# Kernel optimization log

Hardware: AMD Instinct MI355X
Metric: run time of the kernel (lower is better)

## Reference

```python
import jax, jax.numpy as jnp
import numpy as np
from jax import lax

B, N, G, K, D = 32, 32768, 64, 32, 384
EPS = 1e-5


def _fps(xyz, npoint):
    # Farthest point sampling; deterministic start at index 0 (original uses randint).
    b, n, _ = xyz.shape
    def step(carry, _):
        distance, farthest = carry
        centroid = jnp.take_along_axis(xyz, farthest[:, None, None], axis=1)  # (B,1,3)
        dist = jnp.sum((xyz - centroid) ** 2, axis=-1)                        # (B,N)
        distance = jnp.minimum(distance, dist)
        new_far = jnp.argmax(distance, axis=-1)
        return (distance, new_far), farthest
    init = (jnp.full((b, n), 1e10, xyz.dtype), jnp.zeros((b,), jnp.int32))
    _, cents = lax.scan(step, init, None, length=npoint)  # (npoint, B)
    return cents.T  # (B, npoint)


def _bn(h, g, bta, m, v):
    # inference-mode BatchNorm over channel (last) dim
    return (h - m) * (g * lax.rsqrt(v + EPS)) + bta


def setup_inputs() -> dict:
    key = jax.random.key(0)
    ks = jax.random.split(key, 5)
    xyz = jax.random.normal(ks[0], (B, N, 3), jnp.float32)
    features = jax.random.normal(ks[1], (B, N, 3), jnp.float32)
    w1 = jax.random.normal(ks[2], (64, 6), jnp.float32) * 0.1
    w2 = jax.random.normal(ks[3], (128, 64), jnp.float32) * 0.1
    w3 = jax.random.normal(ks[4], (D, 128), jnp.float32) * 0.1
    def bn(c):
        return jnp.ones((c,), jnp.float32), jnp.zeros((c,), jnp.float32), jnp.zeros((c,), jnp.float32), jnp.ones((c,), jnp.float32)
    g1, b1, m1, v1 = bn(64)
    g2, b2, m2, v2 = bn(128)
    g3, b3, m3, v3 = bn(D)
    return dict(xyz=xyz, features=features, w1=w1, g1=g1, b1=b1, m1=m1, v1=v1,
                w2=w2, g2=g2, b2=b2, m2=m2, v2=v2, w3=w3, g3=g3, b3=b3, m3=m3, v3=v3)


def reference(xyz, features, w1, g1, b1, m1, v1, w2, g2, b2, m2, v2, w3, g3, b3, m3, v3):
    fps_idx = _fps(xyz, G)                                           # (B,G)
    center = jnp.take_along_axis(xyz, fps_idx[:, :, None], axis=1)   # (B,G,3)
    # KNN via squared distances (same ordering as torch.cdist euclidean)
    xn2 = jnp.sum(xyz * xyz, axis=-1)                                # (B,N)
    cn2 = jnp.sum(center * center, axis=-1)                          # (B,G)
    d2 = cn2[:, :, None] + xn2[:, None, :] - 2.0 * jnp.einsum('bgc,bnc->bgn', center, xyz)
    _, knn_idx = lax.top_k(-d2, K)                                   # (B,G,K)
    gx = jax.vmap(lambda x, i: x[i])(xyz, knn_idx)                   # (B,G,K,3)
    gf = jax.vmap(lambda f, i: f[i])(features, knn_idx)              # (B,G,K,3)
    h = jnp.concatenate([gx - center[:, :, None, :], gf], axis=-1)   # (B,G,K,6)
    h = jax.nn.relu(_bn(jnp.einsum('bgkc,oc->bgko', h, w1), g1, b1, m1, v1))
    h = jax.nn.relu(_bn(jnp.einsum('bgkc,oc->bgko', h, w2), g2, b2, m2, v2))
    h = _bn(jnp.einsum('bgkc,oc->bgko', h, w3), g3, b3, m3, v3)      # (B,G,K,D)
    patch = jnp.max(h, axis=2)                                       # (B,G,D) adaptive max pool
    return center, patch
```

## Files before the change

### kernel.cpp

```cpp
#include <hip/hip_runtime.h>
#include <hip/hip_bf16.h>

#define BB 32
#define NN 32768
#define GG 64
#define KK 32
#define DD 384
#define EPSF 1e-5f
#define FPS_NBLK 8
#define FPS_SL   (NN/FPS_NBLK)

typedef __attribute__((ext_vector_type(8))) short short8;
typedef __attribute__((ext_vector_type(4))) float f32x4;

__device__ __forceinline__ float rn_add(float a, float b){ return __fadd_rn(a,b); }
__device__ __forceinline__ float rn_sub(float a, float b){ return __fsub_rn(a,b); }
__device__ __forceinline__ float rn_mul(float a, float b){ return __fmul_rn(a,b); }

__device__ __forceinline__ unsigned fkey(float d){
  unsigned u = __float_as_uint(d);
  return (u & 0x80000000u) ? ~u : (u | 0x80000000u);
}

__device__ __forceinline__ unsigned short f2bf(float f){
  unsigned u = __float_as_uint(f);
  unsigned r = (u + 0x7FFFu + ((u >> 16) & 1u)) >> 16;
  return (unsigned short)r;
}

#define REP8(X) X(0) X(1) X(2) X(3) X(4) X(5) X(6) X(7)

__device__ float g_center[BB*GG*3];
__device__ int   g_knn[BB*GG*KK];
__device__ float g_w1t[6*64];
__device__ float g_b1[64];
__device__ float g_b2[128];
__device__ float g_b3[384];
__device__ __align__(16) unsigned short g_w2f[8*2*64*8];
__device__ __align__(16) unsigned short g_w3f[24*4*64*8];
__device__ float g_X[BB*NN];
__device__ float g_Y[BB*NN];
__device__ float g_Z[BB*NN];
__device__ float g_N2[BB*NN];
__device__ unsigned long long g_part[BB*FPS_NBLK*GG];

__global__ __launch_bounds__(256) void k_soa(const float* __restrict__ xyz){
  int tid = blockIdx.x * blockDim.x + threadIdx.x;
  int b = tid >> 15;
  int p = tid & (NN - 1);
  const float* s = xyz + (size_t)b*NN*3 + (size_t)p*3;
  float x = s[0], y = s[1], z = s[2];
  g_X[tid] = x;
  g_Y[tid] = y;
  g_Z[tid] = z;
  g_N2[tid] = rn_add(rn_add(rn_mul(x,x), rn_mul(y,y)), rn_mul(z,z));
}

__global__ __launch_bounds__(256) void k_zero(void){
  int tid = blockIdx.x * blockDim.x + threadIdx.x;
  if (tid < BB*FPS_NBLK*GG) g_part[tid] = 0ull;
}

__global__ void k_prep(const float* __restrict__ w1, const float* __restrict__ g1, const float* __restrict__ b1, const float* __restrict__ m1, const float* __restrict__ v1,
                       const float* __restrict__ w2, const float* __restrict__ g2, const float* __restrict__ b2, const float* __restrict__ m2, const float* __restrict__ v2,
                       const float* __restrict__ w3, const float* __restrict__ g3, const float* __restrict__ b3, const float* __restrict__ m3, const float* __restrict__ v3){
  int tid = blockIdx.x * blockDim.x + threadIdx.x;
  int nt  = gridDim.x * blockDim.x;
  for (int e = tid; e < 64*6; e += nt){
    int c = e >> 6, o = e & 63;
    float s = g1[o] * rsqrtf(v1[o] + EPSF);
    g_w1t[e] = w1[o*6 + c] * s;
  }
  for (int o = tid; o < 64; o += nt){
    float s = g1[o] * rsqrtf(v1[o] + EPSF);
    g_b1[o] = b1[o] - m1[o]*s;
  }
  for (int o = tid; o < 128; o += nt){
    float s = g2[o] * rsqrtf(v2[o] + EPSF);
    g_b2[o] = b2[o] - m2[o]*s;
  }
  for (int o = tid; o < 384; o += nt){
    float s = g3[o] * rsqrtf(v3[o] + EPSF);
    g_b3[o] = b3[o] - m3[o]*s;
  }
  for (int idx = tid; idx < 8192; idx += nt){
    int e  = idx & 7;
    int l  = (idx >> 3) & 63;
    int kt = (idx >> 9) & 1;
    int ct = idx >> 10;
    int j  = ct*16 + (l & 15);
    int k  = kt*32 + ((l >> 4) << 3) + e;
    float s = g2[j] * rsqrtf(v2[j] + EPSF);
    g_w2f[idx] = f2bf(w2[j*64 + k] * s);
  }
  for (int idx = tid; idx < 49152; idx += nt){
    int e  = idx & 7;
    int l  = (idx >> 3) & 63;
    int kt = (idx >> 9) & 3;
    int ct = idx >> 11;
    int j  = ct*16 + (l & 15);
    int k  = kt*32 + ((l >> 4) << 3) + e;
    float s = g3[j] * rsqrtf(v3[j] + EPSF);
    g_w3f[idx] = f2bf(w3[j*128 + k] * s);
  }
}

__global__ __launch_bounds__(512)
void k_fps(float* __restrict__ outCenter){
  const int blk = blockIdx.x;
  const int b   = blk & 31;
  const int sub = blk >> 5;
  const int t   = threadIdx.x;
  const int wv  = t >> 6, ln = t & 63;
  const int base = sub * FPS_SL;
  const float* Xb = g_X + (size_t)b*NN;
  const float* Yb = g_Y + (size_t)b*NN;
  const float* Zb = g_Z + (size_t)b*NN;

  __shared__ float sx[FPS_SL], sy[FPS_SL], szz[FPS_SL];
  __shared__ unsigned long long skey[8];
  __shared__ int s_far;

  #pragma unroll
  for (int i = 0; i < 8; ++i){
    int p = (i << 9) + t;
    sx[p]  = Xb[base + p];
    sy[p]  = Yb[base + p];
    szz[p] = Zb[base + p];
  }
  __syncthreads();

#define DD_DECL(i) float dd##i = 1e10f;
  REP8(DD_DECL)
#undef DD_DECL

  int far = 0;
  for (int it = 0; ; ++it){
    if (sub == 0 && t == 0){
      float cx = Xb[far], cy = Yb[far], cz = Zb[far];
      float* cw = g_center  + (size_t)(b*GG + it)*3;
      float* co = outCenter + (size_t)(b*GG + it)*3;
      cw[0] = cx; cw[1] = cy; cw[2] = cz;
      co[0] = cx; co[1] = cy; co[2] = cz;
    }
    if (it == GG - 1) break;

    float cx = Xb[far], cy = Yb[far], cz = Zb[far];
    unsigned long long bk = 0ull;
#define DD_UPD(i) { \
    int p = (i << 9) + t; \
    float dx = rn_sub(sx[p], cx); \
    float dy = rn_sub(sy[p], cy); \
    float dz = rn_sub(szz[p], cz); \
    float s_ = rn_add(rn_add(rn_mul(dx,dx), rn_mul(dy,dy)), rn_mul(dz,dz)); \
    float d_ = fminf(dd##i, s_); \
    dd##i = d_; \
    unsigned long long k_ = ((unsigned long long)fkey(d_) << 32) \
                          | (unsigned)(0xFFFFFFFFu - (unsigned)(base + p)); \
    if (k_ > bk) bk = k_; }
    REP8(DD_UPD)
#undef DD_UPD

    #pragma unroll
    for (int off = 32; off >= 1; off >>= 1){
      unsigned long long o = (unsigned long long)__shfl_xor((long long)bk, off);
      if (o > bk) bk = o;
    }
    if (ln == 0) skey[wv] = bk;
    __syncthreads();
    if (wv == 0){
      unsigned long long m = (ln < 8) ? skey[ln] : 0ull;
      #pragma unroll
      for (int off = 1; off <= 4; off <<= 1){
        unsigned long long o = (unsigned long long)__shfl_xor((long long)m, off);
        if (o > m) m = o;
      }
      if (ln == 0)
        __hip_atomic_store(&g_part[(((b << 3) + sub) << 6) + it], m,
                           __ATOMIC_RELAXED, __HIP_MEMORY_SCOPE_AGENT);
      unsigned long long k = 0ull;
      if (ln < 8){
        unsigned long long* p = &g_part[(((b << 3) + ln) << 6) + it];
        do {
          k = __hip_atomic_load(p, __ATOMIC_RELAXED, __HIP_MEMORY_SCOPE_AGENT);
        } while (k == 0ull);
      }
      #pragma unroll
      for (int off = 1; off <= 4; off <<= 1){
        unsigned long long o = (unsigned long long)__shfl_xor((long long)k, off);
        if (o > k) k = o;
      }
      if (ln == 0) s_far = (int)(0xFFFFFFFFu - (unsigned)(k & 0xFFFFFFFFu));
    }
    __syncthreads();
    far = s_far;
  }
}

__global__ __launch_bounds__(256) void k_knn(void){
  const int bg = blockIdx.x;
  const int b  = bg >> 6;
  const int t  = threadIdx.x;
  const int w  = t >> 6;
  const int ln = t & 63;
  const float4* X4 = (const float4*)(g_X  + (size_t)b*NN);
  const float4* Y4 = (const float4*)(g_Y  + (size_t)b*NN);
  const float4* Z4 = (const float4*)(g_Z  + (size_t)b*NN);
  const float4* N4 = (const float4*)(g_N2 + (size_t)b*NN);

  __shared__ unsigned sE[64];
  __shared__ unsigned long long s_cand[512];
  __shared__ int s_cnt;

  const float* cp = g_center + (size_t)bg*3;
  float cx = cp[0], cy = cp[1], cz = cp[2];
  float cn2 = rn_add(rn_add(rn_mul(cx,cx), rn_mul(cy,cy)), rn_mul(cz,cz));

  float e0 = INFINITY, e1 = INFINITY;
  #pragma unroll 2
  for (int s = 0; s < 32; ++s){
    int q = (s << 8) + t;
    float4 x = X4[q], y = Y4[q], z = Z4[q], n = N4[q];
    #define D2C(c) { \
      float e = rn_add(rn_add(rn_mul(cx,x.c), rn_mul(cy,y.c)), rn_mul(cz,z.c)); \
      float d = rn_sub(rn_add(cn2, n.c), rn_add(e,e)); \
      if (d < e1){ if (d < e0){ e1 = e0; e0 = d; } else e1 = d; } }
    D2C(x) D2C(y) D2C(z) D2C(w)
    #undef D2C
  }

  {
    unsigned v = fkey(e1);
    #pragma unroll
    for (int k = 2; k <= 64; k <<= 1){
      #pragma unroll
      for (int j = k >> 1; j > 0; j >>= 1){
        unsigned o = (unsigned)__shfl_xor((int)v, j);
        bool keepmin = (((ln & k) == 0) == ((ln & j) == 0));
        unsigned mn = o < v ? o : v;
        unsigned mx = o < v ? v : o;
        v = keepmin ? mn : mx;
      }
    }
    if (ln < 16) sE[w*16 + ln] = v;
  }
  if (t == 0) s_cnt = 0;
  __syncthreads();

  unsigned T;
  {
    unsigned v = sE[ln];
    #pragma unroll
    for (int k = 2; k <= 64; k <<= 1){
      #pragma unroll
      for (int j = k >> 1; j > 0; j >>= 1){
        unsigned o = (unsigned)__shfl_xor((int)v, j);
        bool keepmin = (((ln & k) == 0) == ((ln & j) == 0));
        unsigned mn = o < v ? o : v;
        unsigned mx = o < v ? v : o;
        v = keepmin ? mn : mx;
      }
    }
    T = (unsigned)__shfl((int)v, 15);
  }

  #pragma unroll 2
  for (int s = 0; s < 32; ++s){
    int q = (s << 8) + t;
    float4 x = X4[q], y = Y4[q], z = Z4[q], n = N4[q];
    #define COLC(c, kk) { \
      float e = rn_add(rn_add(rn_mul(cx,x.c), rn_mul(cy,y.c)), rn_mul(cz,z.c)); \
      float d = rn_sub(rn_add(cn2, n.c), rn_add(e,e)); \
      unsigned fk = fkey(d); \
      if (fk <= T){ \
        int p = atomicAdd(&s_cnt, 1); \
        if (p < 512) \
          s_cand[p] = ((unsigned long long)fk << 32) | (unsigned)((q<<2)+kk); } }
    COLC(x,0) COLC(y,1) COLC(z,2) COLC(w,3)
    #undef COLC
  }
  __syncthreads();

  if (w == 0){
    int C = s_cnt; if (C > 512) C = 512;
    int* kout = g_knn + (size_t)bg*KK;
    if (C <= 64){
      unsigned long long kk = (ln < C) ? s_cand[ln] : ~0ull;
      #pragma unroll
      for (int k = 2; k <= 64; k <<= 1){
        #pragma unroll
        for (int j = k >> 1; j > 0; j >>= 1){
          unsigned long long o = (unsigned long long)__shfl_xor((long long)kk, j);
          bool keepmin = (((ln & k) == 0) == ((ln & j) == 0));
          unsigned long long mn = o < kk ? o : kk;
          unsigned long long mx = o < kk ? kk : o;
          kk = keepmin ? mn : mx;
        }
      }
      if (ln < KK) kout[ln] = (int)(kk & 0xffffffffu);
    } else {
      unsigned long long md[8];
      #pragma unroll
      for (int j = 0; j < 8; ++j){
        int e = ln + (j << 6);
        md[j] = (e < C) ? s_cand[e] : ~0ull;
      }
      for (int r = 0; r < KK; ++r){
        unsigned long long bk = md[0];
        #pragma unroll
        for (int j = 1; j < 8; ++j) if (md[j] < bk) bk = md[j];
        #pragma unroll
        for (int off = 32; off >= 1; off >>= 1){
          unsigned long long o = (unsigned long long)__shfl_xor((long long)bk, off);
          if (o < bk) bk = o;
        }
        #pragma unroll
        for (int j = 0; j < 8; ++j) if (md[j] == bk) md[j] = ~0ull;
        if (ln == 0) kout[r] = (int)(bk & 0xffffffffu);
      }
    }
  }
}

__global__ __launch_bounds__(256) void k_mlp(const float* __restrict__ xyz,
                                             const float* __restrict__ feat,
                                             float* __restrict__ outPatch){
  const int bg = blockIdx.x;
  const int b  = bg >> 6;
  const int t  = threadIdx.x;
  const int w  = t >> 6;
  const int ln = t & 63;
  const float* xb = xyz  + (size_t)b*NN*3;
  const float* fb = feat + (size_t)b*NN*3;

  __shared__ float h0[KK][8];
  __shared__ __align__(16) unsigned short h1b[KK][72];
  __shared__ __align__(16) unsigned short h2b[KK][136];

  if (t < KK){
    int idx = g_knn[(size_t)bg*KK + t] & (NN - 1);
    const float* cp = g_center + (size_t)bg*3;
    h0[t][0] = rn_sub(xb[idx*3+0], cp[0]);
    h0[t][1] = rn_sub(xb[idx*3+1], cp[1]);
    h0[t][2] = rn_sub(xb[idx*3+2], cp[2]);
    h0[t][3] = fb[idx*3+0];
    h0[t][4] = fb[idx*3+1];
    h0[t][5] = fb[idx*3+2];
  }
  __syncthreads();

  {
    int p = t >> 3, ob = (t & 7) * 8;
    float acc[8];
    #pragma unroll
    for (int j = 0; j < 8; ++j) acc[j] = g_b1[ob + j];
    #pragma unroll
    for (int c = 0; c < 6; ++c){
      float a = h0[p][c];
      const float4* wr = (const float4*)(g_w1t + c*64 + ob);
      float4 wa = wr[0], wb = wr[1];
      acc[0] = fmaf(a, wa.x, acc[0]); acc[1] = fmaf(a, wa.y, acc[1]);
      acc[2] = fmaf(a, wa.z, acc[2]); acc[3] = fmaf(a, wa.w, acc[3]);
      acc[4] = fmaf(a, wb.x, acc[4]); acc[5] = fmaf(a, wb.y, acc[5]);
      acc[6] = fmaf(a, wb.z, acc[6]); acc[7] = fmaf(a, wb.w, acc[7]);
    }
    short8 v;
    #pragma unroll
    for (int j = 0; j < 8; ++j) v[j] = (short)f2bf(fmaxf(acc[j], 0.f));
    *reinterpret_cast<short8*>(&h1b[p][ob]) = v;
  }
  __syncthreads();

  {
    f32x4 a00 = {0,0,0,0}, a01 = {0,0,0,0}, a10 = {0,0,0,0}, a11 = {0,0,0,0};
    const int g8 = (ln >> 4) << 3;
    #pragma unroll
    for (int kk = 0; kk < 2; ++kk){
      short8 A0 = *reinterpret_cast<const short8*>(&h1b[(ln & 15)][kk*32 + g8]);
      short8 A1 = *reinterpret_cast<const short8*>(&h1b[16 + (ln & 15)][kk*32 + g8]);
      short8 B0 = *reinterpret_cast<const short8*>(&g_w2f[(((2*w+0)*2 + kk)*64 + ln)*8]);
      short8 B1 = *reinterpret_cast<const short8*>(&g_w2f[(((2*w+1)*2 + kk)*64 + ln)*8]);
      a00 = __builtin_amdgcn_mfma_f32_16x16x32_bf16(A0, B0, a00, 0, 0, 0);
      a01 = __builtin_amdgcn_mfma_f32_16x16x32_bf16(A1, B0, a01, 0, 0, 0);
      a10 = __builtin_amdgcn_mfma_f32_16x16x32_bf16(A0, B1, a10, 0, 0, 0);
      a11 = __builtin_amdgcn_mfma_f32_16x16x32_bf16(A1, B1, a11, 0, 0, 0);
    }
    int col0 = (2*w)*16 + (ln & 15);
    int col1 = col0 + 16;
    float bz0 = g_b2[col0], bz1 = g_b2[col1];
    int r0 = (ln >> 4) << 2;
    #pragma unroll
    for (int r = 0; r < 4; ++r){
      h2b[r0 + r][col0]      = f2bf(fmaxf(a00[r] + bz0, 0.f));
      h2b[16 + r0 + r][col0] = f2bf(fmaxf(a01[r] + bz0, 0.f));
      h2b[r0 + r][col1]      = f2bf(fmaxf(a10[r] + bz1, 0.f));
      h2b[16 + r0 + r][col1] = f2bf(fmaxf(a11[r] + bz1, 0.f));
    }
  }
  __syncthreads();

  {
    f32x4 acc3[6][2];
    #pragma unroll
    for (int ci = 0; ci < 6; ++ci){
      acc3[ci][0] = (f32x4){0,0,0,0};
      acc3[ci][1] = (f32x4){0,0,0,0};
    }
    const int g8 = (ln >> 4) << 3;
    #pragma unroll
    for (int kk = 0; kk < 4; ++kk){
      short8 A0 = *reinterpret_cast<const short8*>(&h2b[(ln & 15)][kk*32 + g8]);
      short8 A1 = *reinterpret_cast<const short8*>(&h2b[16 + (ln & 15)][kk*32 + g8]);
      #pragma unroll
      for (int ci = 0; ci < 6; ++ci){
        int ct = w*6 + ci;
        short8 B = *reinterpret_cast<const short8*>(&g_w3f[((ct*4 + kk)*64 + ln)*8]);
        acc3[ci][0] = __builtin_amdgcn_mfma_f32_16x16x32_bf16(A0, B, acc3[ci][0], 0, 0, 0);
        acc3[ci][1] = __builtin_amdgcn_mfma_f32_16x16x32_bf16(A1, B, acc3[ci][1], 0, 0, 0);
      }
    }
    #pragma unroll
    for (int ci = 0; ci < 6; ++ci){
      float m = acc3[ci][0][0];
      #pragma unroll
      for (int r = 1; r < 4; ++r) m = fmaxf(m, acc3[ci][0][r]);
      #pragma unroll
      for (int r = 0; r < 4; ++r) m = fmaxf(m, acc3[ci][1][r]);
      m = fmaxf(m, __shfl_xor(m, 16));
      m = fmaxf(m, __shfl_xor(m, 32));
      if (ln < 16){
        int col = (w*6 + ci)*16 + ln;
        outPatch[(size_t)bg*DD + col] = m + g_b3[col];
      }
    }
  }
}

extern "C" void kernel_launch(void* const* d_in, const int* in_sizes, int n_in,
                              void* d_out, int out_size, void* d_ws, size_t ws_size,
                              hipStream_t stream){
  (void)in_sizes; (void)n_in; (void)out_size; (void)d_ws; (void)ws_size;
  const float* xyz  = (const float*)d_in[0];
  const float* feat = (const float*)d_in[1];
  const float* w1 = (const float*)d_in[2];
  const float* g1 = (const float*)d_in[3];
  const float* b1 = (const float*)d_in[4];
  const float* m1 = (const float*)d_in[5];
  const float* v1 = (const float*)d_in[6];
  const float* w2 = (const float*)d_in[7];
  const float* g2 = (const float*)d_in[8];
  const float* b2 = (const float*)d_in[9];
  const float* m2 = (const float*)d_in[10];
  const float* v2 = (const float*)d_in[11];
  const float* w3 = (const float*)d_in[12];
  const float* g3 = (const float*)d_in[13];
  const float* b3 = (const float*)d_in[14];
  const float* m3 = (const float*)d_in[15];
  const float* v3 = (const float*)d_in[16];
  float* out = (float*)d_out;

  k_prep<<<64, 256, 0, stream>>>(w1,g1,b1,m1,v1, w2,g2,b2,m2,v2, w3,g3,b3,m3,v3);
  k_soa<<<(BB*NN)/256, 256, 0, stream>>>(xyz);
  k_zero<<<64, 256, 0, stream>>>();
  k_fps<<<BB*FPS_NBLK, 512, 0, stream>>>(out);
  k_knn<<<BB*GG, 256, 0, stream>>>();
  k_mlp<<<BB*GG, 256, 0, stream>>>(xyz, feat, out + (size_t)BB*GG*3);
}
```

Before: 267.3 us.

## Process four KNN centers per block to reuse point loads

The KNN kernel now handles four centroids per block, so each point load (X, Y, Z, N2) is reused across four distance computations and the launch drops from 2048 to 512 blocks. A new block-to-batch swizzle interleaves batches so that concurrently resident blocks touch different batches. The branchy top-2 update is replaced with branchless fminf/fmaxf, and each wave does the final top-K selection for one centroid. This cuts global and L2 traffic per centroid, at the cost of more registers, four times the candidate shared memory, and fewer blocks to fill the GPU.

```diff
diff --git a/kernel.cpp b/kernel.cpp
--- a/kernel.cpp
+++ b/kernel.cpp
@@ -198,8 +198,9 @@
 }
 
 __global__ __launch_bounds__(256) void k_knn(void){
-  const int bg = blockIdx.x;
-  const int b  = bg >> 6;
+  const int j  = blockIdx.x;
+  const int b  = (j & 7) + ((j >> 7) << 3);
+  const int g0 = ((j >> 3) & 15) << 2;
   const int t  = threadIdx.x;
   const int w  = t >> 6;
   const int ln = t & 63;
@@ -208,90 +209,118 @@
   const float4* Z4 = (const float4*)(g_Z  + (size_t)b*NN);
   const float4* N4 = (const float4*)(g_N2 + (size_t)b*NN);
 
-  __shared__ unsigned sE[64];
-  __shared__ unsigned long long s_cand[512];
-  __shared__ int s_cnt;
-
-  const float* cp = g_center + (size_t)bg*3;
-  float cx = cp[0], cy = cp[1], cz = cp[2];
-  float cn2 = rn_add(rn_add(rn_mul(cx,cx), rn_mul(cy,cy)), rn_mul(cz,cz));
-
-  float e0 = INFINITY, e1 = INFINITY;
+  __shared__ float sC[4][4];
+  __shared__ unsigned sE[4][64];
+  __shared__ unsigned sTk[4];
+  __shared__ unsigned long long cand[4][512];
+  __shared__ int cnt[4];
+
+  if (t < 4){
+    const float* cp = g_center + (size_t)(b*GG + g0 + t)*3;
+    float x = cp[0], y = cp[1], z = cp[2];
+    sC[0][t] = x; sC[1][t] = y; sC[2][t] = z;
+    sC[3][t] = rn_add(rn_add(rn_mul(x,x), rn_mul(y,y)), rn_mul(z,z));
+    cnt[t] = 0;
+  }
+  __syncthreads();
+
+  float cx[4], cy[4], cz[4], cn[4];
+  #pragma unroll
+  for (int c = 0; c < 4; ++c){
+    cx[c] = sC[0][c]; cy[c] = sC[1][c]; cz[c] = sC[2][c]; cn[c] = sC[3][c];
+  }
+
+  float e0[4], e1[4];
+  #pragma unroll
+  for (int c = 0; c < 4; ++c){ e0[c] = INFINITY; e1[c] = INFINITY; }
   #pragma unroll 2
   for (int s = 0; s < 32; ++s){
     int q = (s << 8) + t;
     float4 x = X4[q], y = Y4[q], z = Z4[q], n = N4[q];
-    #define D2C(c) { \
-      float e = rn_add(rn_add(rn_mul(cx,x.c), rn_mul(cy,y.c)), rn_mul(cz,z.c)); \
-      float d = rn_sub(rn_add(cn2, n.c), rn_add(e,e)); \
-      if (d < e1){ if (d < e0){ e1 = e0; e0 = d; } else e1 = d; } }
-    D2C(x) D2C(y) D2C(z) D2C(w)
-    #undef D2C
-  }
-
-  {
-    unsigned v = fkey(e1);
+    #pragma unroll
+    for (int c = 0; c < 4; ++c){
+      #define P1C(comp) { \
+        float e = rn_add(rn_add(rn_mul(cx[c],x.comp), rn_mul(cy[c],y.comp)), rn_mul(cz[c],z.comp)); \
+        float d = rn_sub(rn_add(cn[c], n.comp), rn_add(e,e)); \
+        float nm2 = fminf(e1[c], fmaxf(e0[c], d)); \
+        e0[c] = fminf(e0[c], d); \
+        e1[c] = nm2; }
+      P1C(x) P1C(y) P1C(z) P1C(w)
+      #undef P1C
+    }
+  }
+
+  #pragma unroll
+  for (int c = 0; c < 4; ++c){
+    unsigned v = fkey(e1[c]);
     #pragma unroll
     for (int k = 2; k <= 64; k <<= 1){
       #pragma unroll
-      for (int j = k >> 1; j > 0; j >>= 1){
-        unsigned o = (unsigned)__shfl_xor((int)v, j);
-        bool keepmin = (((ln & k) == 0) == ((ln & j) == 0));
+      for (int jj = k >> 1; jj > 0; jj >>= 1){
+        unsigned o = (unsigned)__shfl_xor((int)v, jj);
+        bool keepmin = (((ln & k) == 0) == ((ln & jj) == 0));
         unsigned mn = o < v ? o : v;
         unsigned mx = o < v ? v : o;
         v = keepmin ? mn : mx;
       }
     }
-    if (ln < 16) sE[w*16 + ln] = v;
-  }
-  if (t == 0) s_cnt = 0;
-  __syncthreads();
-
-  unsigned T;
+    if (ln < 16) sE[c][w*16 + ln] = v;
+  }
+  __syncthreads();
+
   {
-    unsigned v = sE[ln];
+    unsigned v = sE[w][ln];
     #pragma unroll
     for (int k = 2; k <= 64; k <<= 1){
       #pragma unroll
-      for (int j = k >> 1; j > 0; j >>= 1){
-        unsigned o = (unsigned)__shfl_xor((int)v, j);
-        bool keepmin = (((ln & k) == 0) == ((ln & j) == 0));
+      for (int jj = k >> 1; jj > 0; jj >>= 1){
+        unsigned o = (unsigned)__shfl_xor((int)v, jj);
+        bool keepmin = (((ln & k) == 0) == ((ln & jj) == 0));
         unsigned mn = o < v ? o : v;
         unsigned mx = o < v ? v : o;
         v = keepmin ? mn : mx;
       }
     }
-    T = (unsigned)__shfl((int)v, 15);
-  }
+    unsigned T = (unsigned)__shfl((int)v, 15);
+    if (ln == 0) sTk[w] = T;
+  }
+  __syncthreads();
+
+  unsigned Tr[4];
+  #pragma unroll
+  for (int c = 0; c < 4; ++c) Tr[c] = sTk[c];
 
   #pragma unroll 2
   for (int s = 0; s < 32; ++s){
     int q = (s << 8) + t;
     float4 x = X4[q], y = Y4[q], z = Z4[q], n = N4[q];
-    #define COLC(c, kk) { \
-      float e = rn_add(rn_add(rn_mul(cx,x.c), rn_mul(cy,y.c)), rn_mul(cz,z.c)); \
-      float d = rn_sub(rn_add(cn2, n.c), rn_add(e,e)); \
-      unsigned fk = fkey(d); \
-      if (fk <= T){ \
-        int p = atomicAdd(&s_cnt, 1); \
-        if (p < 512) \
-          s_cand[p] = ((unsigned long long)fk << 32) | (unsigned)((q<<2)+kk); } }
-    COLC(x,0) COLC(y,1) COLC(z,2) COLC(w,3)
-    #undef COLC
-  }
-  __syncthreads();
-
-  if (w == 0){
-    int C = s_cnt; if (C > 512) C = 512;
-    int* kout = g_knn + (size_t)bg*KK;
+    #pragma unroll
+    for (int c = 0; c < 4; ++c){
+      #define P2C(comp, kk) { \
+        float e = rn_add(rn_add(rn_mul(cx[c],x.comp), rn_mul(cy[c],y.comp)), rn_mul(cz[c],z.comp)); \
+        float d = rn_sub(rn_add(cn[c], n.comp), rn_add(e,e)); \
+        unsigned fk = fkey(d); \
+        if (fk <= Tr[c]){ \
+          int p = atomicAdd(&cnt[c], 1); \
+          if (p < 512) \
+            cand[c][p] = ((unsigned long long)fk << 32) | (unsigned)((q<<2)+kk); } }
+      P2C(x,0) P2C(y,1) P2C(z,2) P2C(w,3)
+      #undef P2C
+    }
+  }
+  __syncthreads();
+
+  {
+    int C = cnt[w]; if (C > 512) C = 512;
+    int* kout = g_knn + (size_t)(b*GG + g0 + w)*KK;
     if (C <= 64){
-      unsigned long long kk = (ln < C) ? s_cand[ln] : ~0ull;
+      unsigned long long kk = (ln < C) ? cand[w][ln] : ~0ull;
       #pragma unroll
       for (int k = 2; k <= 64; k <<= 1){
         #pragma unroll
-        for (int j = k >> 1; j > 0; j >>= 1){
-          unsigned long long o = (unsigned long long)__shfl_xor((long long)kk, j);
-          bool keepmin = (((ln & k) == 0) == ((ln & j) == 0));
+        for (int jj = k >> 1; jj > 0; jj >>= 1){
+          unsigned long long o = (unsigned long long)__shfl_xor((long long)kk, jj);
+          bool keepmin = (((ln & k) == 0) == ((ln & jj) == 0));
           unsigned long long mn = o < kk ? o : kk;
           unsigned long long mx = o < kk ? kk : o;
           kk = keepmin ? mn : mx;
@@ -301,21 +330,21 @@
     } else {
       unsigned long long md[8];
       #pragma unroll
-      for (int j = 0; j < 8; ++j){
-        int e = ln + (j << 6);
-        md[j] = (e < C) ? s_cand[e] : ~0ull;
+      for (int jj = 0; jj < 8; ++jj){
+        int e = ln + (jj << 6);
+        md[jj] = (e < C) ? cand[w][e] : ~0ull;
       }
       for (int r = 0; r < KK; ++r){
         unsigned long long bk = md[0];
         #pragma unroll
-        for (int j = 1; j < 8; ++j) if (md[j] < bk) bk = md[j];
+        for (int jj = 1; jj < 8; ++jj) if (md[jj] < bk) bk = md[jj];
         #pragma unroll
         for (int off = 32; off >= 1; off >>= 1){
           unsigned long long o = (unsigned long long)__shfl_xor((long long)bk, off);
           if (o < bk) bk = o;
         }
         #pragma unroll
-        for (int j = 0; j < 8; ++j) if (md[j] == bk) md[j] = ~0ull;
+        for (int jj = 0; jj < 8; ++jj) if (md[jj] == bk) md[jj] = ~0ull;
         if (ln == 0) kout[r] = (int)(bk & 0xffffffffu);
       }
     }
@@ -463,6 +492,6 @@
   k_soa<<<(BB*NN)/256, 256, 0, stream>>>(xyz);
   k_zero<<<64, 256, 0, stream>>>();
   k_fps<<<BB*FPS_NBLK, 512, 0, stream>>>(out);
-  k_knn<<<BB*GG, 256, 0, stream>>>();
+  k_knn<<<512, 256, 0, stream>>>();
   k_mlp<<<BB*GG, 256, 0, stream>>>(xyz, feat, out + (size_t)BB*GG*3);
 }
```

Measured after the change: 246.9 us (median of 2 runs). -7.6%, faster.
